# Optimization experiments

Measured on AMD Instinct MI355X. Metric: run time of the kernel, lower is better.

The kernel has to match this reference:

```python
import jax, jax.numpy as jnp
import numpy as np

FILTER_FACTOR = 10  # init kwarg


def median_filter2d(x, k, padding="REFLECT", constant_values=0.0):
    """Faithful port of tfa.image.median_filter2d for NHWC float input.

    tfa pads with pad_top=(k-1)//2, pad_bottom=k-1-pad_top (same for width),
    extracts k*k patches per pixel/channel, and takes the element that
    tf.nn.top_k(patches, area//2+1)[..., -1] yields, i.e. the value at
    ascending-sorted index (area-1)//2.
    """
    B, H, W, C = x.shape
    pt = (k - 1) // 2
    pb = k - 1 - pt
    mode = {"REFLECT": "reflect", "SYMMETRIC": "symmetric", "CONSTANT": "constant"}[padding]
    if mode == "constant":
        xp = jnp.pad(x, ((0, 0), (pt, pb), (pt, pb), (0, 0)), mode=mode,
                     constant_values=constant_values)
    else:
        xp = jnp.pad(x, ((0, 0), (pt, pb), (pt, pb), (0, 0)), mode=mode)
    # Gather sliding windows via advanced indexing (vectorized, no data loops).
    ih = jnp.arange(H)[:, None] + jnp.arange(k)[None, :]  # (H, k)
    iw = jnp.arange(W)[:, None] + jnp.arange(k)[None, :]  # (W, k)
    rows = xp[:, ih]                 # (B, H, k, Wp, C)
    patches = rows[:, :, :, iw]      # (B, H, k, W, k, C)
    patches = patches.transpose(0, 1, 3, 5, 2, 4).reshape(B, H, W, C, k * k)
    area = k * k
    med = jnp.sort(patches, axis=-1)[..., (area - 1) // 2]  # (B, H, W, C)
    return med


def setup_inputs() -> dict:
    key = jax.random.key(0)
    k1, k2 = jax.random.split(key)
    inputs = jax.random.uniform(k1, (2, 224, 224, 3), dtype=jnp.float32)
    # layer draws blend ~ U[0.1, 1.0)
    blend = jax.random.uniform(k2, (1,), dtype=jnp.float32) * 0.9 + 0.1
    return {"inputs": inputs, "blend": blend}


def reference(inputs, blend):
    # training=True path: median filter then tfa.image.blend(filtered, inputs, blend)
    # blend(image1, image2, f) = image1 + f * (image2 - image1)
    k = inputs.shape[1] // FILTER_FACTOR  # height // filter_factor
    filt = median_filter2d(inputs, k, padding="REFLECT", constant_values=0.0)
    f = blend[0]
    return filt + f * (inputs - filt)
```

## Files before the change

### kernel.cpp

```cpp
#include <hip/hip_runtime.h>


#define HH 224
#define WW 224
#define CHN 3
#define KK 22
#define PT 10
#define AREA (KK * KK)
#define RANK 242
#define PXW 8
#define XGS (WW / PXW)
#define DT 2

#define INFF  __int_as_float(0x7f800000)
#define NINFF __int_as_float(0xff800000)

__device__ __forceinline__ int reflect224(int g) {
    int a = abs(g);
    return min(a, 2 * (HH - 1) - a);
}

__device__ __forceinline__ int count8(const float v[8], float t) {
    int c = 0;
#pragma unroll
    for (int i = 0; i < 8; ++i)
        c += __popcll(__ballot(v[i] < t));
    return c;
}

__device__ __forceinline__ float wave_max(float x) {
#pragma unroll
    for (int off = 32; off > 0; off >>= 1)
        x = fmaxf(x, __shfl_xor(x, off, 64));
    return x;
}

__device__ __forceinline__ float wave_min(float x) {
#pragma unroll
    for (int off = 32; off > 0; off >>= 1)
        x = fminf(x, __shfl_xor(x, off, 64));
    return x;
}

__device__ __forceinline__ void gather(float v[8], const float* __restrict__ img,
                                       const int voff[8], int lane, int x) {
    if (x >= PT && x <= WW - 1 - (KK - 1 - PT)) {
        const float* base = img + (x - PT) * CHN;
#pragma unroll
        for (int i = 0; i < 8; ++i) v[i] = base[voff[i]];
    } else {
#pragma unroll
        for (int i = 0; i < 8; ++i) {
            int s   = i * 64 + lane;
            int se  = min(s, AREA - 1);
            int row = se / KK;
            int col = se - row * KK;
            int gy672 = voff[i] - col * CHN;
            int gx = reflect224(x - PT + col);
            v[i] = img[gy672 + gx * CHN];
        }
    }
    v[7] = (lane < AREA - 448) ? v[7] : INFF;
}

__device__ __forceinline__ float extract_med(float v[8], float t, int C) {
    int d = C - RANK;
    float med = t;
    if (d >= 0) {
        int e = d + 1;
#pragma unroll
        for (int i = 0; i < 8; ++i) v[i] = (v[i] < t) ? v[i] : NINFF;
#pragma unroll 1
        for (int r = 0; r < 300; ++r) {
            float m = fmaxf(fmaxf(fmaxf(v[0], v[1]), fmaxf(v[2], v[3])),
                            fmaxf(fmaxf(v[4], v[5]), fmaxf(v[6], v[7])));
            float M = wave_max(m);
            int q = 0;
#pragma unroll
            for (int i = 0; i < 8; ++i)
                q += __popcll(__ballot(v[i] == M));
            if (e <= q) { med = M; break; }
            e -= q;
#pragma unroll
            for (int i = 0; i < 8; ++i)
                v[i] = (v[i] == M) ? NINFF : v[i];
        }
    } else {
        int e = -d;
#pragma unroll
        for (int i = 0; i < 8; ++i) v[i] = (v[i] >= t) ? v[i] : INFF;
#pragma unroll 1
        for (int r = 0; r < 300; ++r) {
            float m = fminf(fminf(fminf(v[0], v[1]), fminf(v[2], v[3])),
                            fminf(fminf(v[4], v[5]), fminf(v[6], v[7])));
            float M = wave_min(m);
            int q = 0;
#pragma unroll
            for (int i = 0; i < 8; ++i)
                q += __popcll(__ballot(v[i] == M));
            if (e <= q) { med = M; break; }
            e -= q;
#pragma unroll
            for (int i = 0; i < 8; ++i)
                v[i] = (v[i] == M) ? INFF : v[i];
        }
    }
    return med;
}

__global__ __launch_bounds__(256)
void median_blend_kernel(const float* __restrict__ in,
                         const float* __restrict__ blend,
                         float* __restrict__ out) {
    const int lane = threadIdx.x & 63;
    const int wid  = threadIdx.x >> 6;
    const int wg = blockIdx.x * 4 + wid;
    const int xg = wg % XGS;
    const int t1 = wg / XGS;
    const int y  = t1 % HH;
    const int t2 = t1 / HH;
    const int c  = t2 % CHN;
    const int b  = t2 / CHN;

    const float f = blend[0];
    const float* img  = in  + (size_t)b * (HH * WW * CHN) + c;
    float*       outp = out + (size_t)b * (HH * WW * CHN) + c;

    int voff[8];
#pragma unroll
    for (int i = 0; i < 8; ++i) {
        int s   = i * 64 + lane;
        int se  = min(s, AREA - 1);
        int row = se / KK;
        int col = se - row * KK;
        int gy  = reflect224(y - PT + row);
        voff[i] = gy * (WW * CHN) + col * CHN;
    }

    const int x0 = xg * PXW;
    float tprev = 0.5f;

    float vA[8];
    gather(vA, img, voff, lane, x0);

    for (int j = 0; j < PXW; ++j) {
        const int x = x0 + j;

        float vN[8];
        const int xn = (j + 1 < PXW) ? (x + 1) : x;
        gather(vN, img, voff, lane, xn);

        float t = tprev;
        int C = count8(vA, t);
        int d = C - RANK;
        float lo = 0.0f, hi = 1.0f;
        int clo = 0, chi = AREA;
#pragma unroll 1
        for (int it = 0; it < 16; ++it) {
            if (d >= -DT && d <= DT) break;
            if (d > 0) { hi = t; chi = C; }
            else       { lo = t; clo = C; }
            float tn = lo + (hi - lo) * (float)(RANK - clo) *
                       __builtin_amdgcn_rcpf((float)(chi - clo));
            if (!(tn > lo && tn < hi)) {
                tn = 0.5f * (lo + hi);
                if (!(tn > lo && tn < hi)) break;
            }
            t = tn;
            C = count8(vA, t);
            d = C - RANK;
        }

        float med = extract_med(vA, t, C);
        tprev = med;

        const float xc = img[y * (WW * CHN) + x * CHN];
        if (lane == 0)
            outp[y * (WW * CHN) + x * CHN] = med + f * (xc - med);

#pragma unroll
        for (int i = 0; i < 8; ++i) vA[i] = vN[i];
    }
}

extern "C" void kernel_launch(void* const* d_in, const int* in_sizes, int n_in,
                              void* d_out, int out_size, void* d_ws, size_t ws_size,
                              hipStream_t stream) {
    const float* in    = (const float*)d_in[0];
    const float* blend = (const float*)d_in[1];
    float* out = (float*)d_out;

    const int nwaves  = 2 * CHN * HH * XGS;
    const int nblocks = nwaves / 4;
    median_blend_kernel<<<nblocks, 256, 0, stream>>>(in, blend, out);
}
```

Before: 163.6 us.

## Process two output pixels per wave iteration with interleaved search and extraction

Each wave now handles two adjacent pixels at once, interleaving their threshold-search and top-k extraction loops so the independent reductions and shuffles can overlap and hide latency. Extraction is unified into a single max-based loop by sign-flipping values for the lower side. The one-ahead prefetch is replaced by gathering both windows at the start of each pair. This raises register pressure, and each loop runs until the slower of the two pixels finishes.

```diff
diff --git a/kernel.cpp b/kernel.cpp
--- a/kernel.cpp
+++ b/kernel.cpp
@@ -28,20 +28,6 @@
     return c;
 }
 
-__device__ __forceinline__ float wave_max(float x) {
-#pragma unroll
-    for (int off = 32; off > 0; off >>= 1)
-        x = fmaxf(x, __shfl_xor(x, off, 64));
-    return x;
-}
-
-__device__ __forceinline__ float wave_min(float x) {
-#pragma unroll
-    for (int off = 32; off > 0; off >>= 1)
-        x = fminf(x, __shfl_xor(x, off, 64));
-    return x;
-}
-
 __device__ __forceinline__ void gather(float v[8], const float* __restrict__ img,
                                        const int voff[8], int lane, int x) {
     if (x >= PT && x <= WW - 1 - (KK - 1 - PT)) {
@@ -61,51 +47,6 @@
         }
     }
     v[7] = (lane < AREA - 448) ? v[7] : INFF;
-}
-
-__device__ __forceinline__ float extract_med(float v[8], float t, int C) {
-    int d = C - RANK;
-    float med = t;
-    if (d >= 0) {
-        int e = d + 1;
-#pragma unroll
-        for (int i = 0; i < 8; ++i) v[i] = (v[i] < t) ? v[i] : NINFF;
-#pragma unroll 1
-        for (int r = 0; r < 300; ++r) {
-            float m = fmaxf(fmaxf(fmaxf(v[0], v[1]), fmaxf(v[2], v[3])),
-                            fmaxf(fmaxf(v[4], v[5]), fmaxf(v[6], v[7])));
-            float M = wave_max(m);
-            int q = 0;
-#pragma unroll
-            for (int i = 0; i < 8; ++i)
-                q += __popcll(__ballot(v[i] == M));
-            if (e <= q) { med = M; break; }
-            e -= q;
-#pragma unroll
-            for (int i = 0; i < 8; ++i)
-                v[i] = (v[i] == M) ? NINFF : v[i];
-        }
-    } else {
-        int e = -d;
-#pragma unroll
-        for (int i = 0; i < 8; ++i) v[i] = (v[i] >= t) ? v[i] : INFF;
-#pragma unroll 1
-        for (int r = 0; r < 300; ++r) {
-            float m = fminf(fminf(fminf(v[0], v[1]), fminf(v[2], v[3])),
-                            fminf(fminf(v[4], v[5]), fminf(v[6], v[7])));
-            float M = wave_min(m);
-            int q = 0;
-#pragma unroll
-            for (int i = 0; i < 8; ++i)
-                q += __popcll(__ballot(v[i] == M));
-            if (e <= q) { med = M; break; }
-            e -= q;
-#pragma unroll
-            for (int i = 0; i < 8; ++i)
-                v[i] = (v[i] == M) ? INFF : v[i];
-        }
-    }
-    return med;
 }
 
 __global__ __launch_bounds__(256)
@@ -140,46 +81,123 @@
     const int x0 = xg * PXW;
     float tprev = 0.5f;
 
-    float vA[8];
-    gather(vA, img, voff, lane, x0);
-
-    for (int j = 0; j < PXW; ++j) {
-        const int x = x0 + j;
-
-        float vN[8];
-        const int xn = (j + 1 < PXW) ? (x + 1) : x;
-        gather(vN, img, voff, lane, xn);
-
-        float t = tprev;
-        int C = count8(vA, t);
-        int d = C - RANK;
-        float lo = 0.0f, hi = 1.0f;
-        int clo = 0, chi = AREA;
 #pragma unroll 1
-        for (int it = 0; it < 16; ++it) {
-            if (d >= -DT && d <= DT) break;
-            if (d > 0) { hi = t; chi = C; }
-            else       { lo = t; clo = C; }
-            float tn = lo + (hi - lo) * (float)(RANK - clo) *
-                       __builtin_amdgcn_rcpf((float)(chi - clo));
-            if (!(tn > lo && tn < hi)) {
-                tn = 0.5f * (lo + hi);
-                if (!(tn > lo && tn < hi)) break;
-            }
-            t = tn;
-            C = count8(vA, t);
-            d = C - RANK;
-        }
-
-        float med = extract_med(vA, t, C);
-        tprev = med;
-
-        const float xc = img[y * (WW * CHN) + x * CHN];
-        if (lane == 0)
-            outp[y * (WW * CHN) + x * CHN] = med + f * (xc - med);
-
-#pragma unroll
-        for (int i = 0; i < 8; ++i) vA[i] = vN[i];
+    for (int j = 0; j < PXW; j += 2) {
+        const int xA = x0 + j;
+        const int xB = xA + 1;
+
+        float vA[8], vB[8];
+        gather(vA, img, voff, lane, xA);
+        gather(vB, img, voff, lane, xB);
+
+        float tA = tprev, tB = tprev;
+        int CA = count8(vA, tA);
+        int CB = count8(vB, tB);
+        float loA = 0.0f, hiA = 1.0f, loB = 0.0f, hiB = 1.0f;
+        int cloA = 0, chiA = AREA, cloB = 0, chiB = AREA;
+        bool actA = true, actB = true;
+#pragma unroll 1
+        for (int it = 0; it < 16 && (actA || actB); ++it) {
+            if (actA) {
+                int d = CA - RANK;
+                if (d >= -DT && d <= DT) actA = false;
+                else {
+                    if (d > 0) { hiA = tA; chiA = CA; }
+                    else       { loA = tA; cloA = CA; }
+                    float tn = loA + (hiA - loA) * (float)(RANK - cloA) *
+                               __builtin_amdgcn_rcpf((float)(chiA - cloA));
+                    if (!(tn > loA && tn < hiA)) {
+                        tn = 0.5f * (loA + hiA);
+                        if (!(tn > loA && tn < hiA)) actA = false;
+                    }
+                    if (actA) { tA = tn; CA = count8(vA, tA); }
+                }
+            }
+            if (actB) {
+                int d = CB - RANK;
+                if (d >= -DT && d <= DT) actB = false;
+                else {
+                    if (d > 0) { hiB = tB; chiB = CB; }
+                    else       { loB = tB; cloB = CB; }
+                    float tn = loB + (hiB - loB) * (float)(RANK - cloB) *
+                               __builtin_amdgcn_rcpf((float)(chiB - cloB));
+                    if (!(tn > loB && tn < hiB)) {
+                        tn = 0.5f * (loB + hiB);
+                        if (!(tn > loB && tn < hiB)) actB = false;
+                    }
+                    if (actB) { tB = tn; CB = count8(vB, tB); }
+                }
+            }
+        }
+
+        const int dA = CA - RANK, dB = CB - RANK;
+        const bool topA = (dA >= 0), topB = (dB >= 0);
+        int eA = topA ? dA + 1 : -dA;
+        int eB = topB ? dB + 1 : -dB;
+        const int sgnA = topA ? 0 : 0x80000000;
+        const int sgnB = topB ? 0 : 0x80000000;
+#pragma unroll
+        for (int i = 0; i < 8; ++i) {
+            bool ltA = vA[i] < tA;
+            float sA = __int_as_float(__float_as_int(vA[i]) ^ sgnA);
+            vA[i] = (ltA == topA) ? sA : NINFF;
+            bool ltB = vB[i] < tB;
+            float sB = __int_as_float(__float_as_int(vB[i]) ^ sgnB);
+            vB[i] = (ltB == topB) ? sB : NINFF;
+        }
+
+        float medA = tA, medB = tB;
+        bool doneA = false, doneB = false;
+#pragma unroll 1
+        for (int r = 0; r < 300 && !(doneA && doneB); ++r) {
+            float mA = fmaxf(fmaxf(fmaxf(vA[0], vA[1]), fmaxf(vA[2], vA[3])),
+                             fmaxf(fmaxf(vA[4], vA[5]), fmaxf(vA[6], vA[7])));
+            float mB = fmaxf(fmaxf(fmaxf(vB[0], vB[1]), fmaxf(vB[2], vB[3])),
+                             fmaxf(fmaxf(vB[4], vB[5]), fmaxf(vB[6], vB[7])));
+#pragma unroll
+            for (int off = 32; off > 0; off >>= 1) {
+                mA = fmaxf(mA, __shfl_xor(mA, off, 64));
+                mB = fmaxf(mB, __shfl_xor(mB, off, 64));
+            }
+            if (!doneA) {
+                int q = 0;
+#pragma unroll
+                for (int i = 0; i < 8; ++i)
+                    q += __popcll(__ballot(vA[i] == mA));
+                if (eA <= q) {
+                    medA = __int_as_float(__float_as_int(mA) ^ sgnA);
+                    doneA = true;
+                } else {
+                    eA -= q;
+#pragma unroll
+                    for (int i = 0; i < 8; ++i)
+                        vA[i] = (vA[i] == mA) ? NINFF : vA[i];
+                }
+            }
+            if (!doneB) {
+                int q = 0;
+#pragma unroll
+                for (int i = 0; i < 8; ++i)
+                    q += __popcll(__ballot(vB[i] == mB));
+                if (eB <= q) {
+                    medB = __int_as_float(__float_as_int(mB) ^ sgnB);
+                    doneB = true;
+                } else {
+                    eB -= q;
+#pragma unroll
+                    for (int i = 0; i < 8; ++i)
+                        vB[i] = (vB[i] == mB) ? NINFF : vB[i];
+                }
+            }
+        }
+        tprev = medB;
+
+        const float xcA = img[y * (WW * CHN) + xA * CHN];
+        const float xcB = img[y * (WW * CHN) + xB * CHN];
+        if (lane == 0) {
+            outp[y * (WW * CHN) + xA * CHN] = medA + f * (xcA - medA);
+            outp[y * (WW * CHN) + xB * CHN] = medB + f * (xcB - medB);
+        }
     }
 }
 
```

Result: no change. 162.9 us (-0.4%).

## Refine median search with exact-count threshold and step-based extraction

Applied to the files above, without the earlier changes.

Reworks the per-pixel selection search. It now takes a first step from the previous median using a fixed density estimate, and iterates until the count below the threshold equals the rank exactly rather than stopping within a tolerance. The final value is then found with one masked wave max, and a stepping loop replaces the repeated remove-the-max extraction. It also drops the prefetch of the next pixel's window, making the gather synchronous, and launches one wave per 64-thread block instead of four waves per block. Together these aim to cut extraction iterations, at the cost of losing load/compute overlap and possibly running more refinement steps.

```diff
diff --git a/kernel.cpp b/kernel.cpp
--- a/kernel.cpp
+++ b/kernel.cpp
@@ -10,7 +10,7 @@
 #define RANK 242
 #define PXW 8
 #define XGS (WW / PXW)
-#define DT 2
+#define INVD (1.0f / 484.0f)
 
 #define INFF  __int_as_float(0x7f800000)
 #define NINFF __int_as_float(0xff800000)
@@ -28,18 +28,26 @@
     return c;
 }
 
-__device__ __forceinline__ float wave_max(float x) {
+__device__ __forceinline__ float wmax_below(const float v[8], float t) {
+    float m = NINFF;
+#pragma unroll
+    for (int i = 0; i < 8; ++i)
+        m = fmaxf(m, (v[i] < t) ? v[i] : NINFF);
 #pragma unroll
     for (int off = 32; off > 0; off >>= 1)
-        x = fmaxf(x, __shfl_xor(x, off, 64));
-    return x;
+        m = fmaxf(m, __shfl_xor(m, off, 64));
+    return m;
 }
 
-__device__ __forceinline__ float wave_min(float x) {
+__device__ __forceinline__ float wmin_above(const float v[8], float t) {
+    float m = INFF;
+#pragma unroll
+    for (int i = 0; i < 8; ++i)
+        m = fminf(m, (v[i] >= t) ? v[i] : INFF);
 #pragma unroll
     for (int off = 32; off > 0; off >>= 1)
-        x = fminf(x, __shfl_xor(x, off, 64));
-    return x;
+        m = fminf(m, __shfl_xor(m, off, 64));
+    return m;
 }
 
 __device__ __forceinline__ void gather(float v[8], const float* __restrict__ img,
@@ -63,58 +71,12 @@
     v[7] = (lane < AREA - 448) ? v[7] : INFF;
 }
 
-__device__ __forceinline__ float extract_med(float v[8], float t, int C) {
-    int d = C - RANK;
-    float med = t;
-    if (d >= 0) {
-        int e = d + 1;
-#pragma unroll
-        for (int i = 0; i < 8; ++i) v[i] = (v[i] < t) ? v[i] : NINFF;
-#pragma unroll 1
-        for (int r = 0; r < 300; ++r) {
-            float m = fmaxf(fmaxf(fmaxf(v[0], v[1]), fmaxf(v[2], v[3])),
-                            fmaxf(fmaxf(v[4], v[5]), fmaxf(v[6], v[7])));
-            float M = wave_max(m);
-            int q = 0;
-#pragma unroll
-            for (int i = 0; i < 8; ++i)
-                q += __popcll(__ballot(v[i] == M));
-            if (e <= q) { med = M; break; }
-            e -= q;
-#pragma unroll
-            for (int i = 0; i < 8; ++i)
-                v[i] = (v[i] == M) ? NINFF : v[i];
-        }
-    } else {
-        int e = -d;
-#pragma unroll
-        for (int i = 0; i < 8; ++i) v[i] = (v[i] >= t) ? v[i] : INFF;
-#pragma unroll 1
-        for (int r = 0; r < 300; ++r) {
-            float m = fminf(fminf(fminf(v[0], v[1]), fminf(v[2], v[3])),
-                            fminf(fminf(v[4], v[5]), fminf(v[6], v[7])));
-            float M = wave_min(m);
-            int q = 0;
-#pragma unroll
-            for (int i = 0; i < 8; ++i)
-                q += __popcll(__ballot(v[i] == M));
-            if (e <= q) { med = M; break; }
-            e -= q;
-#pragma unroll
-            for (int i = 0; i < 8; ++i)
-                v[i] = (v[i] == M) ? INFF : v[i];
-        }
-    }
-    return med;
-}
-
-__global__ __launch_bounds__(256)
+__global__ __launch_bounds__(64)
 void median_blend_kernel(const float* __restrict__ in,
                          const float* __restrict__ blend,
                          float* __restrict__ out) {
-    const int lane = threadIdx.x & 63;
-    const int wid  = threadIdx.x >> 6;
-    const int wg = blockIdx.x * 4 + wid;
+    const int lane = threadIdx.x;
+    const int wg = blockIdx.x;
     const int xg = wg % XGS;
     const int t1 = wg / XGS;
     const int y  = t1 % HH;
@@ -140,46 +102,65 @@
     const int x0 = xg * PXW;
     float tprev = 0.5f;
 
-    float vA[8];
-    gather(vA, img, voff, lane, x0);
-
+#pragma unroll 1
     for (int j = 0; j < PXW; ++j) {
         const int x = x0 + j;
 
-        float vN[8];
-        const int xn = (j + 1 < PXW) ? (x + 1) : x;
-        gather(vN, img, voff, lane, xn);
+        float v[8];
+        gather(v, img, voff, lane, x);
 
         float t = tprev;
-        int C = count8(vA, t);
-        int d = C - RANK;
+        int C = count8(v, t);
         float lo = 0.0f, hi = 1.0f;
         int clo = 0, chi = AREA;
+        bool exact = (C == RANK);
 #pragma unroll 1
-        for (int it = 0; it < 16; ++it) {
-            if (d >= -DT && d <= DT) break;
+        for (int it = 0; it < 12 && !exact; ++it) {
+            int d = C - RANK;
             if (d > 0) { hi = t; chi = C; }
             else       { lo = t; clo = C; }
-            float tn = lo + (hi - lo) * (float)(RANK - clo) *
-                       __builtin_amdgcn_rcpf((float)(chi - clo));
+            float tn = t + (float)(RANK - C) * INVD;
             if (!(tn > lo && tn < hi)) {
-                tn = 0.5f * (lo + hi);
-                if (!(tn > lo && tn < hi)) break;
+                tn = lo + (hi - lo) * (float)(RANK - clo) *
+                     __builtin_amdgcn_rcpf((float)(chi - clo));
+                if (!(tn > lo && tn < hi)) {
+                    tn = 0.5f * (lo + hi);
+                    if (!(tn > lo && tn < hi)) break;
+                }
             }
             t = tn;
-            C = count8(vA, t);
-            d = C - RANK;
+            C = count8(v, t);
+            exact = (C == RANK);
         }
 
-        float med = extract_med(vA, t, C);
+        float med;
+        if (exact) {
+            med = wmax_below(v, t);
+        } else {
+            med = t;
+#pragma unroll 1
+            for (int r = 0; r < 300; ++r) {
+                int d = C - RANK;
+                if (d == 0) { med = wmax_below(v, t); break; }
+                if (d > 0) {
+                    float M = wmax_below(v, t);
+                    int C2 = count8(v, M);
+                    if (C2 < RANK) { med = M; break; }
+                    t = M; C = C2;
+                } else {
+                    float m = wmin_above(v, t);
+                    float tn = __int_as_float(__float_as_int(m) + 1);
+                    int C2 = count8(v, tn);
+                    if (C2 >= RANK) { med = m; break; }
+                    t = tn; C = C2;
+                }
+            }
+        }
         tprev = med;
 
         const float xc = img[y * (WW * CHN) + x * CHN];
         if (lane == 0)
             outp[y * (WW * CHN) + x * CHN] = med + f * (xc - med);
-
-#pragma unroll
-        for (int i = 0; i < 8; ++i) vA[i] = vN[i];
     }
 }
 
@@ -190,7 +171,6 @@
     const float* blend = (const float*)d_in[1];
     float* out = (float*)d_out;
 
-    const int nwaves  = 2 * CHN * HH * XGS;
-    const int nblocks = nwaves / 4;
-    median_blend_kernel<<<nblocks, 256, 0, stream>>>(in, blend, out);
+    const int nwaves = 2 * CHN * HH * XGS;
+    median_blend_kernel<<<nwaves, 64, 0, stream>>>(in, blend, out);
 }
```

New measurement: 196.5 us. 20.1% more time.
